# Kernel tuning notes

Hardware: AMD Instinct MI355X
Metric: run time of the kernel (lower is better)

The kernel has to match this reference:

```python
import jax, jax.numpy as jnp
import numpy as np

B, N, D, H, M, CD = 2, 2048, 1024, 16, 77, 768
DH = D // H          # head dim 64
FF = 4 * D           # GEGLU hidden 4096
NBITS = 8
EPS = 1e-5


def fake_quant_w(w, n_bits=NBITS):
    """Per-tensor uniform affine INT8 fake-quant (UniformAffineQuantizerINT8) with STE."""
    levels = 2 ** n_bits - 1
    mn = jnp.min(w)
    mx = jnp.max(w)
    delta = (mx - mn) / levels
    zp = jnp.round(-mn / delta)
    wq = jnp.clip(jnp.round(w / delta) + zp, 0, levels)
    wdq = (wq - zp) * delta
    return w + jax.lax.stop_gradient(wdq - w)


def layernorm(x, g, b):
    mu = jnp.mean(x, axis=-1, keepdims=True)
    var = jnp.mean((x - mu) ** 2, axis=-1, keepdims=True)
    return (x - mu) * jax.lax.rsqrt(var + EPS) * g + b


def linear(x, w, b=None):
    y = x @ fake_quant_w(w).T
    return y if b is None else y + b


def cross_attn(x, ctx, qw, kw, vw, ow, ob):
    Bq, Nq, _ = x.shape
    Nk = ctx.shape[1]
    q = linear(x, qw).reshape(Bq, Nq, H, DH)     # b n h d
    k = linear(ctx, kw).reshape(Bq, Nk, H, DH)
    v = linear(ctx, vw).reshape(Bq, Nk, H, DH)
    scale = DH ** -0.5
    sim = jnp.einsum('bihd,bjhd->bhij', q, k) * scale   # [B,H,Nq,Nk]
    attn = jax.nn.softmax(sim, axis=-1)
    out = jnp.einsum('bhij,bjhd->bihd', attn, v).reshape(Bq, Nq, D)
    return linear(out, ow, ob)


def geglu_ff(x, w1, b1, w2, b2):
    h = linear(x, w1, b1)                # [B,N,2*FF]
    hidden, gate = jnp.split(h, 2, axis=-1)
    return linear(hidden * jax.nn.gelu(gate), w2, b2)


def setup_inputs() -> dict:
    key = jax.random.key(0)
    ks = jax.random.split(key, 24)
    W = lambda k, o, i: (jax.random.normal(k, (o, i), jnp.float32) * 0.02)
    return {
        'x': jax.random.normal(ks[0], (B, N, D), jnp.float32),
        'context': jax.random.normal(ks[1], (B, M, CD), jnp.float32),
        'ln1_g': 1.0 + 0.1 * jax.random.normal(ks[2], (D,), jnp.float32),
        'ln1_b': 0.1 * jax.random.normal(ks[3], (D,), jnp.float32),
        'ln2_g': 1.0 + 0.1 * jax.random.normal(ks[4], (D,), jnp.float32),
        'ln2_b': 0.1 * jax.random.normal(ks[5], (D,), jnp.float32),
        'ln3_g': 1.0 + 0.1 * jax.random.normal(ks[6], (D,), jnp.float32),
        'ln3_b': 0.1 * jax.random.normal(ks[7], (D,), jnp.float32),
        'q1_w': W(ks[8], D, D), 'k1_w': W(ks[9], D, D), 'v1_w': W(ks[10], D, D),
        'o1_w': W(ks[11], D, D), 'o1_b': jnp.zeros((D,), jnp.float32),
        'q2_w': W(ks[12], D, D), 'k2_w': W(ks[13], D, CD), 'v2_w': W(ks[14], D, CD),
        'o2_w': W(ks[15], D, D), 'o2_b': jnp.zeros((D,), jnp.float32),
        'ff1_w': W(ks[16], 2 * FF, D), 'ff1_b': jnp.zeros((2 * FF,), jnp.float32),
        'ff2_w': W(ks[17], D, FF), 'ff2_b': jnp.zeros((D,), jnp.float32),
    }


def reference(x, context, ln1_g, ln1_b, ln2_g, ln2_b, ln3_g, ln3_b,
              q1_w, k1_w, v1_w, o1_w, o1_b,
              q2_w, k2_w, v2_w, o2_w, o2_b,
              ff1_w, ff1_b, ff2_w, ff2_b):
    x = cross_attn(layernorm(x, ln1_g, ln1_b), layernorm(x, ln1_g, ln1_b),
                   q1_w, k1_w, v1_w, o1_w, o1_b) + x
    x = cross_attn(layernorm(x, ln2_g, ln2_b), context,
                   q2_w, k2_w, v2_w, o2_w, o2_b) + x
    x = geglu_ff(layernorm(x, ln3_g, ln3_b), ff1_w, ff1_b, ff2_w, ff2_b) + x
    return x
```

## Files before the change

kernel.cpp:

```cpp
#include <hip/hip_runtime.h>
#include <cstdint>
#include <cstddef>

typedef unsigned short ushort_t;
typedef short s16x8 __attribute__((ext_vector_type(8)));
typedef float f32x4 __attribute__((ext_vector_type(4)));
typedef unsigned u32x4 __attribute__((ext_vector_type(4)));

#define MFMA(A,B,C) __builtin_amdgcn_mfma_f32_16x16x32_bf16((A),(B),(C),0,0,0)

__device__ __forceinline__ float b2f(ushort_t h){ return __uint_as_float(((unsigned)h)<<16); }
__device__ __forceinline__ ushort_t f2b(float f){
  unsigned u = __float_as_uint(f);
  u += 0x7FFFu + ((u >> 16) & 1u);
  return (ushort_t)(u >> 16);
}
__device__ __forceinline__ unsigned f2o(float f){
  unsigned u = __float_as_uint(f);
  return (u & 0x80000000u) ? ~u : (u | 0x80000000u);
}
__device__ __forceinline__ float o2f(unsigned u){
  unsigned b = (u & 0x80000000u) ? (u & 0x7FFFFFFFu) : ~u;
  return __uint_as_float(b);
}

struct QT { const float* w[10]; ushort_t* o[10]; int n[10]; float os[10]; };

__global__ void init_k(unsigned* slots){
  int t = threadIdx.x;
  if (t < 20) slots[t] = (t & 1) ? 0u : 0xFFFFFFFFu;
}

__global__ __launch_bounds__(256) void minmax_k(QT qt, unsigned* slots){
  int t = blockIdx.y;
  const float4* w = (const float4*)qt.w[t];
  int n4 = qt.n[t] >> 2;
  float mn = 3.4e38f, mx = -3.4e38f;
  for (int i = blockIdx.x*256 + threadIdx.x; i < n4; i += gridDim.x*256){
    float4 v = w[i];
    mn = fminf(mn, fminf(fminf(v.x, v.y), fminf(v.z, v.w)));
    mx = fmaxf(mx, fmaxf(fmaxf(v.x, v.y), fmaxf(v.z, v.w)));
  }
  #pragma unroll
  for (int o = 1; o < 64; o <<= 1){
    mn = fminf(mn, __shfl_xor(mn, o));
    mx = fmaxf(mx, __shfl_xor(mx, o));
  }
  __shared__ float smn[4], smx[4];
  int wv = threadIdx.x >> 6;
  if ((threadIdx.x & 63) == 0){ smn[wv] = mn; smx[wv] = mx; }
  __syncthreads();
  if (threadIdx.x == 0){
    mn = fminf(fminf(smn[0], smn[1]), fminf(smn[2], smn[3]));
    mx = fmaxf(fmaxf(smx[0], smx[1]), fmaxf(smx[2], smx[3]));
    atomicMin(&slots[2*t], f2o(mn));
    atomicMax(&slots[2*t+1], f2o(mx));
  }
}

__global__ __launch_bounds__(256) void dequant_k(QT qt, const unsigned* __restrict__ slots){
  int t = blockIdx.y;
  float mn = o2f(slots[2*t]), mx = o2f(slots[2*t+1]);
  float delta = (mx - mn) * (1.f/255.f);
  float zp = rintf(-mn / delta);
  float osc = qt.os[t];
  const float4* w = (const float4*)qt.w[t];
  ushort4* o = (ushort4*)qt.o[t];
  int n4 = qt.n[t] >> 2;
  for (int i = blockIdx.x*256 + threadIdx.x; i < n4; i += gridDim.x*256){
    float4 v = w[i];
    ushort4 r;
    float q;
    q = fminf(fmaxf(rintf(v.x/delta) + zp, 0.f), 255.f); r.x = f2b((q - zp)*delta*osc);
    q = fminf(fmaxf(rintf(v.y/delta) + zp, 0.f), 255.f); r.y = f2b((q - zp)*delta*osc);
    q = fminf(fmaxf(rintf(v.z/delta) + zp, 0.f), 255.f); r.z = f2b((q - zp)*delta*osc);
    q = fminf(fmaxf(rintf(v.w/delta) + zp, 0.f), 255.f); r.w = f2b((q - zp)*delta*osc);
    o[i] = r;
  }
}

__global__ __launch_bounds__(256) void f2b_k(const float* __restrict__ in, ushort_t* __restrict__ out, int n4){
  for (int i = blockIdx.x*256 + threadIdx.x; i < n4; i += gridDim.x*256){
    float4 v = ((const float4*)in)[i];
    ushort4 r; r.x = f2b(v.x); r.y = f2b(v.y); r.z = f2b(v.z); r.w = f2b(v.w);
    ((ushort4*)out)[i] = r;
  }
}

__global__ __launch_bounds__(256) void ln_k(const float* __restrict__ x, const float* __restrict__ g,
                                            const float* __restrict__ b, ushort_t* __restrict__ out){
  int row = blockIdx.x, tid = threadIdx.x;
  float4 v = ((const float4*)(x + (size_t)row*1024))[tid];
  float s  = v.x + v.y + v.z + v.w;
  float s2 = v.x*v.x + v.y*v.y + v.z*v.z + v.w*v.w;
  #pragma unroll
  for (int o = 1; o < 64; o <<= 1){ s += __shfl_xor(s, o); s2 += __shfl_xor(s2, o); }
  __shared__ float rs[4], rs2[4];
  int wv = tid >> 6;
  if ((tid & 63) == 0){ rs[wv] = s; rs2[wv] = s2; }
  __syncthreads();
  s = rs[0]+rs[1]+rs[2]+rs[3]; s2 = rs2[0]+rs2[1]+rs2[2]+rs2[3];
  float mu = s * (1.f/1024.f);
  float var = s2 * (1.f/1024.f) - mu*mu;
  float rstd = rsqrtf(var + 1e-5f);
  float4 gv = ((const float4*)g)[tid], bv = ((const float4*)b)[tid];
  ushort4 r;
  r.x = f2b((v.x - mu)*rstd*gv.x + bv.x);
  r.y = f2b((v.y - mu)*rstd*gv.y + bv.y);
  r.z = f2b((v.z - mu)*rstd*gv.z + bv.z);
  r.w = f2b((v.w - mu)*rstd*gv.w + bv.w);
  ((ushort4*)(out + (size_t)row*1024))[tid] = r;
}

__global__ __launch_bounds__(512) void gemm_k(
    const ushort_t* __restrict__ A, const ushort_t* __restrict__ W,
    const float* __restrict__ bias, const float* __restrict__ resid,
    float* __restrict__ outF, ushort_t* __restrict__ outB,
    int M, int N, int K, int lda, int ldw)
{
  __shared__ ushort_t As[3][256*32];
  __shared__ ushort_t Bs[3][128*32];
  const int tid = threadIdx.x;
  const int lane = tid & 63, wv = tid >> 6;
  const int g = lane >> 4, qi = lane & 15;

  const int gx = gridDim.x, gy = gridDim.y;
  const int lid = blockIdx.x + blockIdx.y * gx;
  int m0, n0;
  if (((gx & 3) | (gy & 1)) == 0){
    const int w = gx >> 2, h = gy >> 1;
    const int xcd = lid & 7, o = lid >> 3;
    const int cx = xcd & 3, cy = xcd >> 2;
    n0 = (cx * w + (o % w)) * 128;
    m0 = (cy * h + (o / w)) * 256;
  } else {
    n0 = blockIdx.x * 128;
    m0 = blockIdx.y * 256;
  }

  const int koff = blockIdx.z * K;
  if (gridDim.z > 1) outF += (size_t)blockIdx.z * M * N;

  const int wr = (wv >> 1) * 64, wc = (wv & 1) * 64;
  f32x4 acc[4][4] = {};

  const int ra0 = tid >> 2,        sa0 = (tid & 3) ^ ((ra0 >> 1) & 3);
  const int ra1 = (512+tid) >> 2,  sa1 = ((512+tid) & 3) ^ ((ra1 >> 1) & 3);
  const int aA0 = (m0 + ra0 < M) ? m0 + ra0 : M - 1;
  const int aA1 = (m0 + ra1 < M) ? m0 + ra1 : M - 1;
  const size_t dA0 = (size_t)tid*8, dA1 = (size_t)(512+tid)*8, dB0 = (size_t)tid*8;

  #define GSTAGE(bi_, kt_) do {                                                    \
    __builtin_amdgcn_global_load_lds(                                              \
      (const __attribute__((address_space(1))) void*)(A + (size_t)aA0*lda + koff + (kt_) + sa0*8), \
      (__attribute__((address_space(3))) void*)(&As[bi_][dA0]), 16, 0, 0);         \
    __builtin_amdgcn_global_load_lds(                                              \
      (const __attribute__((address_space(1))) void*)(A + (size_t)aA1*lda + koff + (kt_) + sa1*8), \
      (__attribute__((address_space(3))) void*)(&As[bi_][dA1]), 16, 0, 0);         \
    __builtin_amdgcn_global_load_lds(                                              \
      (const __attribute__((address_space(1))) void*)(W + (size_t)(n0 + ra0)*ldw + koff + (kt_) + sa0*8), \
      (__attribute__((address_space(3))) void*)(&Bs[bi_][dB0]), 16, 0, 0);         \
  } while(0)

  const int nt = K >> 5;
  GSTAGE(0, 0);
  if (nt > 1) GSTAGE(1, 32);
  if (nt > 1) asm volatile("s_waitcnt vmcnt(3)" ::: "memory");
  else        asm volatile("s_waitcnt vmcnt(0)" ::: "memory");
  __builtin_amdgcn_s_barrier();
  __builtin_amdgcn_sched_barrier(0);

  int bi = 0;
  for (int t = 0; t < nt; ++t){
    int b2 = bi + 2; if (b2 >= 3) b2 -= 3;
    if (t + 2 < nt) GSTAGE(b2, (t + 2) << 5);
    s16x8 af[4], bfr[4];
    #pragma unroll
    for (int mi = 0; mi < 4; ++mi){
      int row = wr + mi*16 + qi;
      int sl = g ^ ((row >> 1) & 3);
      af[mi] = *(const s16x8*)(&As[bi][row*32 + sl*8]);
    }
    #pragma unroll
    for (int ni = 0; ni < 4; ++ni){
      int row = wc + ni*16 + qi;
      int sl = g ^ ((row >> 1) & 3);
      bfr[ni] = *(const s16x8*)(&Bs[bi][row*32 + sl*8]);
    }
    __builtin_amdgcn_s_setprio(1);
    #pragma unroll
    for (int mi = 0; mi < 4; ++mi)
      #pragma unroll
      for (int ni = 0; ni < 4; ++ni)
        acc[mi][ni] = MFMA(af[mi], bfr[ni], acc[mi][ni]);
    __builtin_amdgcn_s_setprio(0);
    if (t + 1 < nt){
      if (t + 2 < nt) asm volatile("s_waitcnt vmcnt(3)" ::: "memory");
      else            asm volatile("s_waitcnt vmcnt(0)" ::: "memory");
      __builtin_amdgcn_s_barrier();
      __builtin_amdgcn_sched_barrier(0);
    }
    bi += 1; if (bi >= 3) bi -= 3;
  }
  #undef GSTAGE

  #pragma unroll
  for (int mi = 0; mi < 4; ++mi){
    #pragma unroll
    for (int r = 0; r < 4; ++r){
      int row = m0 + wr + mi*16 + g*4 + r;
      if (row >= M) continue;
      #pragma unroll
      for (int ni = 0; ni < 4; ++ni){
        int col = n0 + wc + ni*16 + qi;
        float v = acc[mi][ni][r];
        if (bias)  v += bias[col];
        if (resid) v += resid[(size_t)row*N + col];
        if (outF)  outF[(size_t)row*N + col] = v;
        else       outB[(size_t)row*N + col] = f2b(v);
      }
    }
  }
}

__global__ __launch_bounds__(256) void reduce_k(const float* __restrict__ p0, const float* __restrict__ p1,
                                                const float* __restrict__ bias, const float* __restrict__ resid,
                                                float* __restrict__ outF, ushort_t* __restrict__ outB, int n4){
  for (int i = blockIdx.x*256 + threadIdx.x; i < n4; i += gridDim.x*256){
    float4 a = ((const float4*)p0)[i];
    float4 b = ((const float4*)p1)[i];
    float4 v;
    v.x = a.x + b.x; v.y = a.y + b.y; v.z = a.z + b.z; v.w = a.w + b.w;
    if (bias){
      float4 bb = ((const float4*)bias)[i & 255];
      v.x += bb.x; v.y += bb.y; v.z += bb.z; v.w += bb.w;
    }
    if (resid){
      float4 r = ((const float4*)resid)[i];
      v.x += r.x; v.y += r.y; v.z += r.z; v.w += r.w;
    }
    if (outF) ((float4*)outF)[i] = v;
    else {
      ushort4 o; o.x = f2b(v.x); o.y = f2b(v.y); o.z = f2b(v.z); o.w = f2b(v.w);
      ((ushort4*)outB)[i] = o;
    }
  }
}

__global__ __launch_bounds__(256) void reduce4_k(const float* __restrict__ p0, const float* __restrict__ p1,
                                                 const float* __restrict__ p2, const float* __restrict__ p3,
                                                 const float* __restrict__ bias, const float* __restrict__ resid,
                                                 float* __restrict__ outF, int n4){
  for (int i = blockIdx.x*256 + threadIdx.x; i < n4; i += gridDim.x*256){
    float4 a = ((const float4*)p0)[i];
    float4 b = ((const float4*)p1)[i];
    float4 c = ((const float4*)p2)[i];
    float4 d = ((const float4*)p3)[i];
    float4 r = ((const float4*)resid)[i];
    float4 bb = ((const float4*)bias)[i & 255];
    float4 v;
    v.x = (a.x + b.x) + (c.x + d.x) + r.x + bb.x;
    v.y = (a.y + b.y) + (c.y + d.y) + r.y + bb.y;
    v.z = (a.z + b.z) + (c.z + d.z) + r.z + bb.z;
    v.w = (a.w + b.w) + (c.w + d.w) + r.w + bb.w;
    ((float4*)outF)[i] = v;
  }
}

__global__ __launch_bounds__(256) void vtrans_k(const ushort_t* __restrict__ src, ushort_t* __restrict__ dst,
                                                int rows, int stride, int col_off, int nk_pad){
  __shared__ ushort_t ldst[64*130];
  int n0 = blockIdx.x * 128;
  int b = blockIdx.y >> 4, h = blockIdx.y & 15;
  const ushort_t* s = src + (size_t)b*rows*stride + col_off + h*64;
  for (int idx = threadIdx.x; idx < 128*64; idx += 256){
    int n = idx >> 6, d = idx & 63;
    int ng = n0 + n;
    ushort_t v = (ng < rows) ? s[(size_t)ng*stride + d] : (ushort_t)0;
    ldst[d*130 + n] = v;
  }
  __syncthreads();
  ushort_t* o = dst + (size_t)(b*16 + h)*64*nk_pad;
  for (int idx = threadIdx.x; idx < 64*128; idx += 256){
    int d = idx >> 7, n = idx & 127;
    if (n0 + n < nk_pad) o[(size_t)d*nk_pad + n0 + n] = ldst[d*130 + n];
  }
}

__global__ __launch_bounds__(512) void attn_k(
    const ushort_t* __restrict__ Q, const ushort_t* __restrict__ Kp, const ushort_t* __restrict__ Vt,
    ushort_t* __restrict__ O, int nq, int nk, int qstride, int kvstride, int nk_pad)
{
  __shared__ ushort_t Ks[2][32*64];
  __shared__ ushort_t Vs[2][64*32];
  const int tid = threadIdx.x, lane = tid & 63, wv = tid >> 6;
  const int g = lane >> 4, qi = lane & 15;
  const int b = blockIdx.y >> 4, h = blockIdx.y & 15;
  const int q0 = blockIdx.x*128 + wv*16;

  const ushort_t* Qr = Q + (size_t)(b*nq + q0 + qi)*qstride + h*64;
  s16x8 qf0 = *(const s16x8*)(Qr + g*8);
  s16x8 qf1 = *(const s16x8*)(Qr + 32 + g*8);
  const ushort_t* Kb = Kp + (size_t)b*nk*kvstride + h*64;
  const ushort_t* Vb = Vt + (size_t)(b*16 + h)*64*nk_pad;

  const int krow = (wv & 3)*8 + (lane >> 3);
  const int kgsl = (lane & 7) ^ (krow & 7);
  const int vrow = (wv & 3)*16 + (lane >> 2);
  const int vgsl = (lane & 3) ^ ((vrow >> 1) & 3);

  #define STAGE(buf, kb_) do {                                                   \
    if (wv < 4){                                                                 \
      int kr_ = (kb_) + krow; if (kr_ >= nk) kr_ = nk - 1;                       \
      __builtin_amdgcn_global_load_lds(                                          \
        (const __attribute__((address_space(1))) void*)(Kb + (size_t)kr_*kvstride + kgsl*8), \
        (__attribute__((address_space(3))) void*)(&Ks[buf][(size_t)(wv&3)*512]), 16, 0, 0); \
    } else {                                                                     \
      __builtin_amdgcn_global_load_lds(                                          \
        (const __attribute__((address_space(1))) void*)(Vb + (size_t)vrow*nk_pad + (kb_) + vgsl*8), \
        (__attribute__((address_space(3))) void*)(&Vs[buf][(size_t)(wv&3)*512]), 16, 0, 0); \
    }                                                                            \
  } while(0)

  const int nkp = (nk + 31) & ~31;
  f32x4 ot[4] = {};
  float m_run = -1e30f, l_run = 0.f;

  const int ks0 = (g     ^ (qi & 7)) * 8;
  const int ks1 = ((4+g) ^ (qi & 7)) * 8;
  const int vs0 = (g ^ ((qi >> 1) & 3)) * 8;

  STAGE(0, 0);
  asm volatile("s_waitcnt vmcnt(0)" ::: "memory");
  __syncthreads();
  int cur = 0;
  for (int kb = 0; kb < nkp; kb += 32){
    if (kb + 32 < nkp) STAGE(cur^1, kb + 32);
    s16x8 ka0 = *(const s16x8*)(&Ks[cur][(qi)*64      + ks0]);
    s16x8 ka1 = *(const s16x8*)(&Ks[cur][(qi)*64      + ks1]);
    s16x8 kb0 = *(const s16x8*)(&Ks[cur][(16+qi)*64   + ks0]);
    s16x8 kb1 = *(const s16x8*)(&Ks[cur][(16+qi)*64   + ks1]);
    s16x8 vf0 = *(const s16x8*)(&Vs[cur][(qi)*32      + vs0]);
    s16x8 vf1 = *(const s16x8*)(&Vs[cur][(16+qi)*32   + vs0]);
    s16x8 vf2 = *(const s16x8*)(&Vs[cur][(32+qi)*32   + vs0]);
    s16x8 vf3 = *(const s16x8*)(&Vs[cur][(48+qi)*32   + vs0]);

    f32x4 st0 = {}, st1 = {};
    st0 = MFMA(ka0, qf0, st0);
    st0 = MFMA(ka1, qf1, st0);
    st1 = MFMA(kb0, qf0, st1);
    st1 = MFMA(kb1, qf1, st1);
    float s[8];
    #pragma unroll
    for (int r = 0; r < 4; ++r){ s[r] = st0[r]; s[4+r] = st1[r]; }
    if (kb + 32 > nk){
      #pragma unroll
      for (int r = 0; r < 4; ++r){
        if (kb + 4*g + r >= nk)      s[r]   = -1e30f;
        if (kb + 16 + 4*g + r >= nk) s[4+r] = -1e30f;
      }
    }
    float bm = fmaxf(fmaxf(fmaxf(s[0], s[1]), fmaxf(s[2], s[3])),
                     fmaxf(fmaxf(s[4], s[5]), fmaxf(s[6], s[7])));
    bm = fmaxf(bm, __shfl_xor(bm, 16));
    bm = fmaxf(bm, __shfl_xor(bm, 32));
    if (!__all(bm <= m_run)){
      float m_new = fmaxf(m_run, bm);
      float fac = __builtin_amdgcn_exp2f(m_run - m_new);
      l_run *= fac;
      #pragma unroll
      for (int dd = 0; dd < 4; ++dd)
        #pragma unroll
        for (int r = 0; r < 4; ++r) ot[dd][r] *= fac;
      m_run = m_new;
    }
    float p[8], rsum = 0.f;
    #pragma unroll
    for (int i = 0; i < 8; ++i){ p[i] = __builtin_amdgcn_exp2f(s[i] - m_run); rsum += p[i]; }
    rsum += __shfl_xor(rsum, 16);
    rsum += __shfl_xor(rsum, 32);
    l_run += rsum;
    unsigned pk[4];
    #pragma unroll
    for (int r = 0; r < 4; ++r)
      pk[r] = (unsigned)f2b(p[r]) | ((unsigned)f2b(p[4+r]) << 16);
    int srcbase = ((2*g) & 3) * 16 + qi;
    unsigned sh0[4], sh1[4];
    #pragma unroll
    for (int r = 0; r < 4; ++r){
      sh0[r] = (unsigned)__shfl((int)pk[r], srcbase);
      sh1[r] = (unsigned)__shfl((int)pk[r], srcbase + 16);
    }
    unsigned sel = (g >> 1) ? 0x07060302u : 0x05040100u;
    u32x4 pw;
    pw[0] = __builtin_amdgcn_perm(sh0[1], sh0[0], sel);
    pw[1] = __builtin_amdgcn_perm(sh0[3], sh0[2], sel);
    pw[2] = __builtin_amdgcn_perm(sh1[1], sh1[0], sel);
    pw[3] = __builtin_amdgcn_perm(sh1[3], sh1[2], sel);
    s16x8 pf = __builtin_bit_cast(s16x8, pw);
    ot[0] = MFMA(vf0, pf, ot[0]);
    ot[1] = MFMA(vf1, pf, ot[1]);
    ot[2] = MFMA(vf2, pf, ot[2]);
    ot[3] = MFMA(vf3, pf, ot[3]);

    asm volatile("s_waitcnt vmcnt(0)" ::: "memory");
    __syncthreads();
    cur ^= 1;
  }
  #undef STAGE
  float inv = 1.f / l_run;
  ushort_t* Or = O + (size_t)(b*nq + q0 + qi)*1024 + h*64;
  #pragma unroll
  for (int dd = 0; dd < 4; ++dd)
    #pragma unroll
    for (int r = 0; r < 4; ++r)
      Or[dd*16 + 4*g + r] = f2b(ot[dd][r] * inv);
}

__global__ __launch_bounds__(256) void geglu_k(const ushort_t* __restrict__ h, ushort_t* __restrict__ out){
  int idx = blockIdx.x*256 + threadIdx.x;
  int r = idx >> 9, c = idx & 511;
  s16x8 hv = *(const s16x8*)(h + (size_t)r*8192 + c*8);
  s16x8 gv = *(const s16x8*)(h + (size_t)r*8192 + 4096 + c*8);
  s16x8 o;
  #pragma unroll
  for (int i = 0; i < 8; ++i){
    float gg = b2f((ushort_t)gv[i]);
    float t  = 0.7978845608f*(gg + 0.044715f*gg*gg*gg);
    float e  = __expf(2.f*t);
    float th = 1.f - 2.f/(e + 1.f);
    float ge = 0.5f*gg*(1.f + th);
    o[i] = (short)f2b(b2f((ushort_t)hv[i]) * ge);
  }
  *(s16x8*)(out + (size_t)r*4096 + c*8) = o;
}

extern "C" void kernel_launch(void* const* d_in, const int* in_sizes, int n_in,
                              void* d_out, int out_size, void* d_ws, size_t ws_size,
                              hipStream_t stream)
{
  const float* x    = (const float*)d_in[0];
  const float* ctx  = (const float*)d_in[1];
  const float* ln1g = (const float*)d_in[2];
  const float* ln1b = (const float*)d_in[3];
  const float* ln2g = (const float*)d_in[4];
  const float* ln2b = (const float*)d_in[5];
  const float* ln3g = (const float*)d_in[6];
  const float* ln3b = (const float*)d_in[7];
  const float* q1w  = (const float*)d_in[8];
  const float* k1w  = (const float*)d_in[9];
  const float* v1w  = (const float*)d_in[10];
  const float* o1w  = (const float*)d_in[11];
  const float* o1b  = (const float*)d_in[12];
  const float* q2w  = (const float*)d_in[13];
  const float* k2w  = (const float*)d_in[14];
  const float* v2w  = (const float*)d_in[15];
  const float* o2w  = (const float*)d_in[16];
  const float* o2b  = (const float*)d_in[17];
  const float* ff1w = (const float*)d_in[18];
  const float* ff1b = (const float*)d_in[19];
  const float* ff2w = (const float*)d_in[20];
  const float* ff2b = (const float*)d_in[21];

  char* base = (char*)d_ws;
  size_t off = 0;
  auto alloc = [&](size_t bytes) -> char* {
    char* p = base + off;
    off += (bytes + 255) & ~(size_t)255;
    return p;
  };
  unsigned*  slots = (unsigned*)alloc(80);
  ushort_t*  ctxb  = (ushort_t*)alloc((size_t)154*768*2);
  ushort_t*  wqkv1 = (ushort_t*)alloc((size_t)3072*1024*2);
  ushort_t*  o1d   = (ushort_t*)alloc((size_t)1024*1024*2);
  ushort_t*  q2d   = (ushort_t*)alloc((size_t)1024*1024*2);
  ushort_t*  wkv2  = (ushort_t*)alloc((size_t)2048*768*2);
  ushort_t*  o2d   = (ushort_t*)alloc((size_t)1024*1024*2);
  ushort_t*  f1d   = (ushort_t*)alloc((size_t)8192*1024*2);
  ushort_t*  f2d   = (ushort_t*)alloc((size_t)1024*4096*2);
  ushort_t*  lnb   = (ushort_t*)alloc((size_t)4096*1024*2);
  ushort_t*  qkvb  = (ushort_t*)alloc((size_t)4096*3072*2);
  ushort_t*  q2b   = (ushort_t*)alloc((size_t)4096*1024*2);
  ushort_t*  atb   = (ushort_t*)alloc((size_t)4096*1024*2);
  ushort_t*  kvb   = (ushort_t*)alloc((size_t)154*2048*2);
  ushort_t*  vt1   = (ushort_t*)alloc((size_t)2*16*64*2048*2);
  ushort_t*  vt2   = (ushort_t*)alloc((size_t)2*16*64*96*2);
  float*     x1    = (float*)alloc((size_t)4096*1024*4);
  float*     x2    = (float*)alloc((size_t)4096*1024*4);
  ushort_t*  hb    = (ushort_t*)alloc((size_t)4096*8192*2);
  ushort_t*  actb  = qkvb;
  float*     part  = (float*)hb;
  float*     part1 = part + (size_t)4096*1024;
  float*     part2 = part + (size_t)2*4096*1024;
  float*     part3 = part + (size_t)3*4096*1024;

  const float SC = 0.18033688011f;
  QT qt;
  qt.w[0]=q1w;  qt.o[0]=wqkv1;               qt.n[0]=1024*1024; qt.os[0]=SC;
  qt.w[1]=k1w;  qt.o[1]=wqkv1+1024*1024;     qt.n[1]=1024*1024; qt.os[1]=1.f;
  qt.w[2]=v1w;  qt.o[2]=wqkv1+2*1024*1024;   qt.n[2]=1024*1024; qt.os[2]=1.f;
  qt.w[3]=o1w;  qt.o[3]=o1d;                 qt.n[3]=1024*1024; qt.os[3]=1.f;
  qt.w[4]=q2w;  qt.o[4]=q2d;                 qt.n[4]=1024*1024; qt.os[4]=SC;
  qt.w[5]=k2w;  qt.o[5]=wkv2;                qt.n[5]=1024*768;  qt.os[5]=1.f;
  qt.w[6]=v2w;  qt.o[6]=wkv2+1024*768;       qt.n[6]=1024*768;  qt.os[6]=1.f;
  qt.w[7]=o2w;  qt.o[7]=o2d;                 qt.n[7]=1024*1024; qt.os[7]=1.f;
  qt.w[8]=ff1w; qt.o[8]=f1d;                 qt.n[8]=8192*1024; qt.os[8]=1.f;
  qt.w[9]=ff2w; qt.o[9]=f2d;                 qt.n[9]=1024*4096; qt.os[9]=1.f;

  init_k<<<1, 64, 0, stream>>>(slots);
  minmax_k<<<dim3(64,10), 256, 0, stream>>>(qt, slots);
  dequant_k<<<dim3(64,10), 256, 0, stream>>>(qt, slots);
  f2b_k<<<64, 256, 0, stream>>>(ctx, ctxb, 154*768/4);

  ln_k<<<4096, 256, 0, stream>>>(x, ln1g, ln1b, lnb);
  gemm_k<<<dim3(24, 16), 512, 0, stream>>>(lnb, wqkv1, nullptr, nullptr,
                                           nullptr, qkvb, 4096, 3072, 1024, 1024, 1024);
  vtrans_k<<<dim3(16, 32), 256, 0, stream>>>(qkvb, vt1, 2048, 3072, 2048, 2048);
  attn_k<<<dim3(16, 32), 512, 0, stream>>>(qkvb, qkvb+1024, vt1, atb,
                                           2048, 2048, 3072, 3072, 2048);
  gemm_k<<<dim3(8, 16, 2), 512, 0, stream>>>(atb, o1d, nullptr, nullptr,
                                             part, nullptr, 4096, 1024, 512, 1024, 1024);
  reduce_k<<<2048, 256, 0, stream>>>(part, part1, o1b, x, x1, nullptr, 4096*1024/4);

  ln_k<<<4096, 256, 0, stream>>>(x1, ln2g, ln2b, lnb);
  gemm_k<<<dim3(8, 16, 2), 512, 0, stream>>>(lnb, q2d, nullptr, nullptr,
                                             part, nullptr, 4096, 1024, 512, 1024, 1024);
  reduce_k<<<2048, 256, 0, stream>>>(part, part1, nullptr, nullptr, nullptr, q2b, 4096*1024/4);
  gemm_k<<<dim3(16, 1), 512, 0, stream>>>(ctxb, wkv2, nullptr, nullptr,
                                          nullptr, kvb, 154, 2048, 768, 768, 768);
  vtrans_k<<<dim3(1, 32), 256, 0, stream>>>(kvb, vt2, 77, 2048, 1024, 96);
  attn_k<<<dim3(16, 32), 512, 0, stream>>>(q2b, kvb, vt2, atb,
                                           2048, 77, 1024, 2048, 96);
  gemm_k<<<dim3(8, 16, 2), 512, 0, stream>>>(atb, o2d, nullptr, nullptr,
                                             part, nullptr, 4096, 1024, 512, 1024, 1024);
  reduce_k<<<2048, 256, 0, stream>>>(part, part1, o2b, x1, x2, nullptr, 4096*1024/4);

  ln_k<<<4096, 256, 0, stream>>>(x2, ln3g, ln3b, lnb);
  gemm_k<<<dim3(64, 16), 512, 0, stream>>>(lnb, f1d, ff1b, nullptr,
                                           nullptr, hb, 4096, 8192, 1024, 1024, 1024);
  geglu_k<<<8192, 256, 0, stream>>>(hb, actb);
  gemm_k<<<dim3(8, 16, 4), 512, 0, stream>>>(actb, f2d, nullptr, nullptr,
                                             part, nullptr, 4096, 1024, 1024, 4096, 4096);
  reduce4_k<<<2048, 256, 0, stream>>>(part, part1, part2, part3, ff2b, x2,
                                      (float*)d_out, 4096*1024/4);
}
```

Measured before the change: 598.8 us.

## Fuse GEGLU activation into FF1 GEMM epilogue via interleaved weight rows

The dequant kernel now writes the FF1 weight rows interleaved in 64-row groups, so each 128-column output tile of the FF1 GEMM holds matching hidden and gate columns. A dedicated FF1 GEMM kernel exchanges the gate half through shared memory and applies bias and tanh-GELU gating in its epilogue, writing the 4096-wide activation directly. This removes the 8192-wide bf16 intermediate write and read and the separate geglu launch. The cost is an extra LDS round trip in the epilogue, and half of the waves sit idle while the output is written.

```diff
diff --git a/kernel.cpp b/kernel.cpp
--- a/kernel.cpp
+++ b/kernel.cpp
@@ -24,7 +24,7 @@
   return __uint_as_float(b);
 }
 
-struct QT { const float* w[10]; ushort_t* o[10]; int n[10]; float os[10]; };
+struct QT { const float* w[10]; ushort_t* o[10]; int n[10]; float os[10]; int pm[10]; };
 
 __global__ void init_k(unsigned* slots){
   int t = threadIdx.x;
@@ -64,6 +64,7 @@
   float delta = (mx - mn) * (1.f/255.f);
   float zp = rintf(-mn / delta);
   float osc = qt.os[t];
+  int pm = qt.pm[t];
   const float4* w = (const float4*)qt.w[t];
   ushort4* o = (ushort4*)qt.o[t];
   int n4 = qt.n[t] >> 2;
@@ -75,7 +76,14 @@
     q = fminf(fmaxf(rintf(v.y/delta) + zp, 0.f), 255.f); r.y = f2b((q - zp)*delta*osc);
     q = fminf(fmaxf(rintf(v.z/delta) + zp, 0.f), 255.f); r.z = f2b((q - zp)*delta*osc);
     q = fminf(fmaxf(rintf(v.w/delta) + zp, 0.f), 255.f); r.w = f2b((q - zp)*delta*osc);
-    o[i] = r;
+    size_t oi = i;
+    if (pm){
+      int row = i >> 8, c4 = i & 255;
+      int nr = (row < 4096) ? ((row >> 6) << 7) + (row & 63)
+                            : (((row - 4096) >> 6) << 7) + 64 + ((row - 4096) & 63);
+      oi = (size_t)nr*256 + c4;
+    }
+    o[oi] = r;
   }
 }
 
@@ -223,6 +231,126 @@
   }
 }
 
+__global__ __launch_bounds__(512) void gemm_ff1_k(
+    const ushort_t* __restrict__ A, const ushort_t* __restrict__ W,
+    const float* __restrict__ biasHG, ushort_t* __restrict__ out)
+{
+  __shared__ union SM {
+    struct { ushort_t As[3][256*32]; ushort_t Bs[3][128*32]; } p;
+    float gbuf[4*64*65];
+  } sm;
+  const int tid = threadIdx.x;
+  const int lane = tid & 63, wv = tid >> 6;
+  const int g = lane >> 4, qi = lane & 15;
+  const int M = 4096, lda = 1024, ldw = 1024;
+
+  const int gx = gridDim.x;
+  const int gy = gridDim.y;
+  const int lid = blockIdx.x + blockIdx.y * gx;
+  const int w = gx >> 2, h = gy >> 1;
+  const int xcd = lid & 7, o = lid >> 3;
+  const int cx = xcd & 3, cy = xcd >> 2;
+  const int n0 = (cx * w + (o % w)) * 128;
+  const int m0 = (cy * h + (o / w)) * 256;
+
+  const int wr = (wv >> 1) * 64, wc = (wv & 1) * 64;
+  f32x4 acc[4][4] = {};
+
+  const int ra0 = tid >> 2,        sa0 = (tid & 3) ^ ((ra0 >> 1) & 3);
+  const int ra1 = (512+tid) >> 2,  sa1 = ((512+tid) & 3) ^ ((ra1 >> 1) & 3);
+  const int aA0 = m0 + ra0, aA1 = m0 + ra1;
+  const size_t dA0 = (size_t)tid*8, dA1 = (size_t)(512+tid)*8, dB0 = (size_t)tid*8;
+
+  #define GSTAGEF(bi_, kt_) do {                                                   \
+    __builtin_amdgcn_global_load_lds(                                              \
+      (const __attribute__((address_space(1))) void*)(A + (size_t)aA0*lda + (kt_) + sa0*8), \
+      (__attribute__((address_space(3))) void*)(&sm.p.As[bi_][dA0]), 16, 0, 0);    \
+    __builtin_amdgcn_global_load_lds(                                              \
+      (const __attribute__((address_space(1))) void*)(A + (size_t)aA1*lda + (kt_) + sa1*8), \
+      (__attribute__((address_space(3))) void*)(&sm.p.As[bi_][dA1]), 16, 0, 0);    \
+    __builtin_amdgcn_global_load_lds(                                              \
+      (const __attribute__((address_space(1))) void*)(W + (size_t)(n0 + ra0)*ldw + (kt_) + sa0*8), \
+      (__attribute__((address_space(3))) void*)(&sm.p.Bs[bi_][dB0]), 16, 0, 0);    \
+  } while(0)
+
+  const int nt = 1024 >> 5;
+  GSTAGEF(0, 0);
+  GSTAGEF(1, 32);
+  asm volatile("s_waitcnt vmcnt(3)" ::: "memory");
+  __builtin_amdgcn_s_barrier();
+  __builtin_amdgcn_sched_barrier(0);
+
+  int bi = 0;
+  for (int t = 0; t < nt; ++t){
+    int b2 = bi + 2; if (b2 >= 3) b2 -= 3;
+    if (t + 2 < nt) GSTAGEF(b2, (t + 2) << 5);
+    s16x8 af[4], bfr[4];
+    #pragma unroll
+    for (int mi = 0; mi < 4; ++mi){
+      int row = wr + mi*16 + qi;
+      int sl = g ^ ((row >> 1) & 3);
+      af[mi] = *(const s16x8*)(&sm.p.As[bi][row*32 + sl*8]);
+    }
+    #pragma unroll
+    for (int ni = 0; ni < 4; ++ni){
+      int row = wc + ni*16 + qi;
+      int sl = g ^ ((row >> 1) & 3);
+      bfr[ni] = *(const s16x8*)(&sm.p.Bs[bi][row*32 + sl*8]);
+    }
+    __builtin_amdgcn_s_setprio(1);
+    #pragma unroll
+    for (int mi = 0; mi < 4; ++mi)
+      #pragma unroll
+      for (int ni = 0; ni < 4; ++ni)
+        acc[mi][ni] = MFMA(af[mi], bfr[ni], acc[mi][ni]);
+    __builtin_amdgcn_s_setprio(0);
+    if (t + 1 < nt){
+      if (t + 2 < nt) asm volatile("s_waitcnt vmcnt(3)" ::: "memory");
+      else            asm volatile("s_waitcnt vmcnt(0)" ::: "memory");
+      __builtin_amdgcn_s_barrier();
+      __builtin_amdgcn_sched_barrier(0);
+    }
+    bi += 1; if (bi >= 3) bi -= 3;
+  }
+  #undef GSTAGEF
+
+  const int jb = n0 >> 1;
+  float* gt = sm.gbuf + (size_t)(wv >> 1) * 64 * 65;
+  __syncthreads();
+  if (wv & 1){
+    #pragma unroll
+    for (int mi = 0; mi < 4; ++mi)
+      #pragma unroll
+      for (int r = 0; r < 4; ++r){
+        int lr = mi*16 + g*4 + r;
+        #pragma unroll
+        for (int ni = 0; ni < 4; ++ni)
+          gt[lr*65 + ni*16 + qi] = acc[mi][ni][r];
+      }
+  }
+  __syncthreads();
+  if (!(wv & 1)){
+    #pragma unroll
+    for (int mi = 0; mi < 4; ++mi)
+      #pragma unroll
+      for (int r = 0; r < 4; ++r){
+        int lr = mi*16 + g*4 + r;
+        int row = m0 + wr + lr;
+        #pragma unroll
+        for (int ni = 0; ni < 4; ++ni){
+          int lc = ni*16 + qi;
+          float hv = acc[mi][ni][r] + biasHG[jb + lc];
+          float gg = gt[lr*65 + lc]  + biasHG[4096 + jb + lc];
+          float tt = 0.7978845608f*(gg + 0.044715f*gg*gg*gg);
+          float e  = __builtin_amdgcn_exp2f(2.885390082f*tt);
+          float th = 1.f - 2.f/(e + 1.f);
+          float ge = 0.5f*gg*(1.f + th);
+          out[(size_t)row*4096 + jb + lc] = f2b(hv * ge);
+        }
+      }
+  }
+}
+
 __global__ __launch_bounds__(256) void reduce_k(const float* __restrict__ p0, const float* __restrict__ p1,
                                                 const float* __restrict__ bias, const float* __restrict__ resid,
                                                 float* __restrict__ outF, ushort_t* __restrict__ outB, int n4){
@@ -415,24 +543,6 @@
     #pragma unroll
     for (int r = 0; r < 4; ++r)
       Or[dd*16 + 4*g + r] = f2b(ot[dd][r] * inv);
-}
-
-__global__ __launch_bounds__(256) void geglu_k(const ushort_t* __restrict__ h, ushort_t* __restrict__ out){
-  int idx = blockIdx.x*256 + threadIdx.x;
-  int r = idx >> 9, c = idx & 511;
-  s16x8 hv = *(const s16x8*)(h + (size_t)r*8192 + c*8);
-  s16x8 gv = *(const s16x8*)(h + (size_t)r*8192 + 4096 + c*8);
-  s16x8 o;
-  #pragma unroll
-  for (int i = 0; i < 8; ++i){
-    float gg = b2f((ushort_t)gv[i]);
-    float t  = 0.7978845608f*(gg + 0.044715f*gg*gg*gg);
-    float e  = __expf(2.f*t);
-    float th = 1.f - 2.f/(e + 1.f);
-    float ge = 0.5f*gg*(1.f + th);
-    o[i] = (short)f2b(b2f((ushort_t)hv[i]) * ge);
-  }
-  *(s16x8*)(out + (size_t)r*4096 + c*8) = o;
 }
 
 extern "C" void kernel_launch(void* const* d_in, const int* in_sizes, int n_in,
@@ -496,16 +606,16 @@
 
   const float SC = 0.18033688011f;
   QT qt;
-  qt.w[0]=q1w;  qt.o[0]=wqkv1;               qt.n[0]=1024*1024; qt.os[0]=SC;
-  qt.w[1]=k1w;  qt.o[1]=wqkv1+1024*1024;     qt.n[1]=1024*1024; qt.os[1]=1.f;
-  qt.w[2]=v1w;  qt.o[2]=wqkv1+2*1024*1024;   qt.n[2]=1024*1024; qt.os[2]=1.f;
-  qt.w[3]=o1w;  qt.o[3]=o1d;                 qt.n[3]=1024*1024; qt.os[3]=1.f;
-  qt.w[4]=q2w;  qt.o[4]=q2d;                 qt.n[4]=1024*1024; qt.os[4]=SC;
-  qt.w[5]=k2w;  qt.o[5]=wkv2;                qt.n[5]=1024*768;  qt.os[5]=1.f;
-  qt.w[6]=v2w;  qt.o[6]=wkv2+1024*768;       qt.n[6]=1024*768;  qt.os[6]=1.f;
-  qt.w[7]=o2w;  qt.o[7]=o2d;                 qt.n[7]=1024*1024; qt.os[7]=1.f;
-  qt.w[8]=ff1w; qt.o[8]=f1d;                 qt.n[8]=8192*1024; qt.os[8]=1.f;
-  qt.w[9]=ff2w; qt.o[9]=f2d;                 qt.n[9]=1024*4096; qt.os[9]=1.f;
+  qt.w[0]=q1w;  qt.o[0]=wqkv1;               qt.n[0]=1024*1024; qt.os[0]=SC;  qt.pm[0]=0;
+  qt.w[1]=k1w;  qt.o[1]=wqkv1+1024*1024;     qt.n[1]=1024*1024; qt.os[1]=1.f; qt.pm[1]=0;
+  qt.w[2]=v1w;  qt.o[2]=wqkv1+2*1024*1024;   qt.n[2]=1024*1024; qt.os[2]=1.f; qt.pm[2]=0;
+  qt.w[3]=o1w;  qt.o[3]=o1d;                 qt.n[3]=1024*1024; qt.os[3]=1.f; qt.pm[3]=0;
+  qt.w[4]=q2w;  qt.o[4]=q2d;                 qt.n[4]=1024*1024; qt.os[4]=SC;  qt.pm[4]=0;
+  qt.w[5]=k2w;  qt.o[5]=wkv2;                qt.n[5]=1024*768;  qt.os[5]=1.f; qt.pm[5]=0;
+  qt.w[6]=v2w;  qt.o[6]=wkv2+1024*768;       qt.n[6]=1024*768;  qt.os[6]=1.f; qt.pm[6]=0;
+  qt.w[7]=o2w;  qt.o[7]=o2d;                 qt.n[7]=1024*1024; qt.os[7]=1.f; qt.pm[7]=0;
+  qt.w[8]=ff1w; qt.o[8]=f1d;                 qt.n[8]=8192*1024; qt.os[8]=1.f; qt.pm[8]=1;
+  qt.w[9]=ff2w; qt.o[9]=f2d;                 qt.n[9]=1024*4096; qt.os[9]=1.f; qt.pm[9]=0;
 
   init_k<<<1, 64, 0, stream>>>(slots);
   minmax_k<<<dim3(64,10), 256, 0, stream>>>(qt, slots);
@@ -536,9 +646,7 @@
   reduce_k<<<2048, 256, 0, stream>>>(part, part1, o2b, x1, x2, nullptr, 4096*1024/4);
 
   ln_k<<<4096, 256, 0, stream>>>(x2, ln3g, ln3b, lnb);
-  gemm_k<<<dim3(64, 16), 512, 0, stream>>>(lnb, f1d, ff1b, nullptr,
-                                           nullptr, hb, 4096, 8192, 1024, 1024, 1024);
-  geglu_k<<<8192, 256, 0, stream>>>(hb, actb);
+  gemm_ff1_k<<<dim3(64, 16), 512, 0, stream>>>(lnb, f1d, ff1b, actb);
   gemm_k<<<dim3(8, 16, 4), 512, 0, stream>>>(actb, f2d, nullptr, nullptr,
                                              part, nullptr, 4096, 1024, 1024, 4096, 4096);
   reduce4_k<<<2048, 256, 0, stream>>>(part, part1, part2, part3, ff2b, x2,
```

New measurement: 619.9 us. 3.5% more time.
